# Optimization experiments

Measured on AMD Instinct MI355X. Metric: run time of the kernel, lower is better.

Reference implementation:

```python
import jax, jax.numpy as jnp
import numpy as np

N_WORDS = 30000
EMB_DIM = 784  # 28*28
MAT_DIM = 28
BATCH = 1024
SEQ_LEN = 64


def setup_inputs() -> dict:
    key = jax.random.key(0)
    k_sent, k_tab = jax.random.split(key)
    # token ids in [0, n_words]; row 0 is the neutral (identity) / padding element
    sent = jax.random.randint(k_sent, (BATCH, SEQ_LEN), 0, N_WORDS + 1, dtype=jnp.int32).astype(jnp.int64)
    eye_flat = jnp.eye(MAT_DIM, dtype=jnp.float32).reshape(-1)
    # 'identity' init strategy: identity + small gaussian noise (scale kept small for stability of long products)
    table = eye_flat + 0.01 * jax.random.normal(k_tab, (N_WORDS + 1, EMB_DIM), dtype=jnp.float32)
    table = table.at[0].set(eye_flat)  # neutral element at padding_idx=0
    return {"sent": sent, "table": table}


def reference(sent, table):
    # sent: [B, S] int ids; table: [n_words+1, d*d]
    B, S = sent.shape
    d = MAT_DIM
    word_mats = table[sent].reshape(B, S, d, d)  # embedding lookup + unflatten
    # CMOW: continual multiplication cur = cur @ W_i, sequential over seq dim
    init = word_mats[:, 0]                      # [B, d, d]
    rest = jnp.moveaxis(word_mats[:, 1:], 1, 0)  # [S-1, B, d, d]

    def step(cur, w):
        return jnp.matmul(cur, w), None

    cur, _ = jax.lax.scan(step, init, rest)
    return cur.reshape(B, d * d)  # flatten matrix back to embedding
```

## Files before the change

### kernel.cpp

```cpp
#include <hip/hip_runtime.h>
#include <stdint.h>

#define SEQ 64
#define D 28
#define EMB 784
#define NW 4
#define CH 16
#define BUFF 832
#define SCRW 36

typedef float float4v __attribute__((ext_vector_type(4)));
typedef __bf16 bf16x8 __attribute__((ext_vector_type(8)));

union FragU { unsigned u[4]; bf16x8 v; };

__device__ __forceinline__ unsigned fbits(float x) { union { float f; unsigned u; } t; t.f = x; return t.u; }
__device__ __forceinline__ float fof(unsigned u) { union { unsigned u; float f; } t; t.u = u; return t.f; }

struct HL4 { unsigned h01, h23, l01, l23; };
__device__ __forceinline__ HL4 hilo4(float x0, float x1, float x2, float x3) {
    unsigned u0 = fbits(x0), u1 = fbits(x1), u2 = fbits(x2), u3 = fbits(x3);
    HL4 r;
    r.h01 = (u0 >> 16) | (u1 & 0xFFFF0000u);
    r.h23 = (u2 >> 16) | (u3 & 0xFFFF0000u);
    unsigned l0 = fbits(x0 - fof(u0 & 0xFFFF0000u));
    unsigned l1 = fbits(x1 - fof(u1 & 0xFFFF0000u));
    unsigned l2 = fbits(x2 - fof(u2 & 0xFFFF0000u));
    unsigned l3 = fbits(x3 - fof(u3 & 0xFFFF0000u));
    r.l01 = (l0 >> 16) | (l1 & 0xFFFF0000u);
    r.l23 = (l2 >> 16) | (l3 & 0xFFFF0000u);
    return r;
}

__device__ __forceinline__ void dma_row(const float* grow, float* lbuf, int lane)
{
    const char* g16 = (const char*)grow + lane * 16;
    const char* g4  = (const char*)grow + 3072 + lane * 4;
    char* l = (char*)lbuf;
    __builtin_amdgcn_global_load_lds((const __attribute__((address_space(1))) void*)(g16),
                                     (__attribute__((address_space(3))) void*)(l), 16, 0, 0);
    __builtin_amdgcn_global_load_lds((const __attribute__((address_space(1))) void*)(g16 + 1024),
                                     (__attribute__((address_space(3))) void*)(l + 1024), 16, 0, 0);
    __builtin_amdgcn_global_load_lds((const __attribute__((address_space(1))) void*)(g16 + 2048),
                                     (__attribute__((address_space(3))) void*)(l + 2048), 16, 0, 0);
    __builtin_amdgcn_global_load_lds((const __attribute__((address_space(1))) void*)(g4),
                                     (__attribute__((address_space(3))) void*)(l + 3072), 4, 0, 0);
}

template<int STRIDE>
__device__ __forceinline__ void stepT(const float* a0, const float* a1,
                                      float4v acc[2][2], bool q3)
{
    float av[2][2][4];
#pragma unroll
    for (int t = 0; t < 4; ++t)
#pragma unroll
        for (int Ro = 0; Ro < 2; ++Ro) {
            av[Ro][0][t] = a0[t * STRIDE + 16 * Ro];
            av[Ro][1][t] = a1[t * STRIDE + 16 * Ro];
        }
#pragma unroll
    for (int Ro = 0; Ro < 2; ++Ro)
#pragma unroll
        for (int t = 0; t < 4; ++t)
            av[Ro][1][t] = q3 ? 0.f : av[Ro][1][t];

    FragU Af[2][2];
#pragma unroll
    for (int Ro = 0; Ro < 2; ++Ro)
#pragma unroll
        for (int KB = 0; KB < 2; ++KB) {
            HL4 h = hilo4(av[Ro][KB][0], av[Ro][KB][1], av[Ro][KB][2], av[Ro][KB][3]);
            Af[Ro][KB].u[0] = h.h01; Af[Ro][KB].u[1] = h.h23;
            Af[Ro][KB].u[2] = h.l01; Af[Ro][KB].u[3] = h.l23;
        }

    FragU Bd[2][2], B2[2][2];
#pragma unroll
    for (int KB = 0; KB < 2; ++KB)
#pragma unroll
        for (int Co = 0; Co < 2; ++Co) {
            HL4 h = hilo4(acc[KB][Co][0], acc[KB][Co][1], acc[KB][Co][2], acc[KB][Co][3]);
            Bd[KB][Co].u[0] = h.h01; Bd[KB][Co].u[1] = h.h23;
            Bd[KB][Co].u[2] = h.h01; Bd[KB][Co].u[3] = h.h23;
            B2[KB][Co].u[0] = h.l01; B2[KB][Co].u[1] = h.l23;
            B2[KB][Co].u[2] = 0u;    B2[KB][Co].u[3] = 0u;
        }

#pragma unroll
    for (int Ro = 0; Ro < 2; ++Ro)
#pragma unroll
        for (int Co = 0; Co < 2; ++Co) {
            float4v d = {0.f, 0.f, 0.f, 0.f};
#pragma unroll
            for (int KB = 0; KB < 2; ++KB) {
                d = __builtin_amdgcn_mfma_f32_16x16x32_bf16(Af[Ro][KB].v, Bd[KB][Co].v, d, 0, 0, 0);
                d = __builtin_amdgcn_mfma_f32_16x16x32_bf16(Af[Ro][KB].v, B2[KB][Co].v, d, 0, 0, 0);
            }
            acc[Ro][Co] = d;
        }
}

__global__ __launch_bounds__(NW * 64, 4) void w2m_fusedT3(
    const int* __restrict__ sent,
    const float* __restrict__ table,
    float* __restrict__ out)
{
    __shared__ float SH[NW * 3 * BUFF] __attribute__((aligned(16)));
    const int lane = threadIdx.x & 63;
    const int wid  = threadIdx.x >> 6;
    const int b = blockIdx.x;
    const int c = lane & 15;
    const int quad = lane >> 4;
    const bool q3 = (quad == 3);
    const int qc = q3 ? 2 : quad;

    float* B0 = &SH[wid * 3 * BUFF];
    float* B1 = B0 + BUFF;
    float* B2b = B0 + 2 * BUFF;

    const int myidx = sent[b * SEQ + CH * wid + (lane & (CH - 1))];
    int jl[CH];
#pragma unroll
    for (int j = 0; j < CH; ++j) jl[j] = __builtin_amdgcn_readlane(myidx, j);

    dma_row(table + (size_t)jl[0] * EMB, B0, lane);
    dma_row(table + (size_t)jl[1] * EMB, B1, lane);
    dma_row(table + (size_t)jl[2] * EMB, B2b, lane);
    __builtin_amdgcn_s_waitcnt(0x0078);

    float4v acc[2][2];
#pragma unroll
    for (int R = 0; R < 2; ++R)
#pragma unroll
        for (int Cc = 0; Cc < 2; ++Cc) {
            int rcl = 16 * Cc + c; if (rcl > 27) rcl = 27;
            acc[R][Cc] = *(const float4v*)&B0[rcl * D + 16 * R + 4 * quad];
        }

    const float* a00 = B0  + 4 * quad * D + c;
    const float* a10 = B0  + (16 + 4 * qc) * D + c;
    const float* a01 = B1  + 4 * quad * D + c;
    const float* a11 = B1  + (16 + 4 * qc) * D + c;
    const float* a02 = B2b + 4 * quad * D + c;
    const float* a12 = B2b + (16 + 4 * qc) * D + c;

#pragma unroll
    for (int j = 1; j < CH; ++j) {
        __builtin_amdgcn_s_waitcnt(0xC07F);
        const int jn = (j + 2 < CH) ? j + 2 : CH - 1;
        const int tb = (j + 2) % 3;
        float* nB = (tb == 0) ? B0 : (tb == 1) ? B1 : B2b;
        dma_row(table + (size_t)jl[jn] * EMB, nB, lane);

        __builtin_amdgcn_sched_barrier(0);
        __builtin_amdgcn_s_waitcnt(0x0078);
        __builtin_amdgcn_sched_barrier(0);

        const int cb = j % 3;
        if (cb == 0)      stepT<D>(a00, a10, acc, q3);
        else if (cb == 1) stepT<D>(a01, a11, acc, q3);
        else              stepT<D>(a02, a12, acc, q3);
    }

    __builtin_amdgcn_s_waitcnt(0x0070);
    __builtin_amdgcn_sched_barrier(0);
    float* SCR = B0;
#pragma unroll
    for (int R = 0; R < 2; ++R)
#pragma unroll
        for (int Cc = 0; Cc < 2; ++Cc)
#pragma unroll
            for (int i = 0; i < 4; ++i)
                SCR[(16 * R + 4 * quad + i) * SCRW + 16 * Cc + c] = acc[R][Cc][i];
    __syncthreads();

    const float* S3 = &SH[3 * 3 * BUFF];
#pragma unroll
    for (int R = 0; R < 2; ++R)
#pragma unroll
        for (int Cc = 0; Cc < 2; ++Cc)
            acc[R][Cc] = *(const float4v*)&S3[(16 * Cc + c) * SCRW + 16 * R + 4 * quad];

#pragma unroll
    for (int j = 2; j >= 0; --j) {
        const float* reg = &SH[j * 3 * BUFF];
        stepT<SCRW>(reg + 4 * quad * SCRW + c,
                    reg + (16 + 4 * quad) * SCRW + c, acc, q3);
    }

    if (wid == 0) {
        float* orow = out + (size_t)b * EMB;
#pragma unroll
        for (int R = 0; R < 2; ++R)
#pragma unroll
            for (int Cc = 0; Cc < 2; ++Cc)
#pragma unroll
                for (int i = 0; i < 4; ++i) {
                    const int row = 16 * R + 4 * quad + i;
                    const int col = 16 * Cc + c;
                    if (row < D && col < D) orow[row * D + col] = acc[R][Cc][i];
                }
    }
}

extern "C" void kernel_launch(void* const* d_in, const int* in_sizes, int n_in,
                              void* d_out, int out_size, void* d_ws, size_t ws_size,
                              hipStream_t stream) {
    const int* sent = (const int*)d_in[0];
    const float* table = (const float*)d_in[1];
    float* out = (float*)d_out;
    const int batch = in_sizes[0] / SEQ;
    (void)d_ws; (void)ws_size;

    hipLaunchKernelGGL(w2m_fusedT3, dim3(batch), dim3(NW * 64), 0, stream,
                       sent, table, out);
}
```

Baseline: 153.3 us.

## Interleave two independent product chains per wave to break MFMA dependency

Each wave's 16-matrix chunk is split into two independent chains, the first eight and last eight matrices, with token loads interleaved so consecutive steps alternate between two accumulators. The two partial products are then combined through LDS before the existing cross-wave reduction. The aim is to hide MFMA and conversion latency in the serial matmul chain by giving the scheduler independent work. The cost is extra registers for the second accumulator and an additional LDS round-trip plus matmul at the end.

Result: no change. 154.0 us (+0.5%).

```diff
diff --git a/kernel.cpp b/kernel.cpp
--- a/kernel.cpp
+++ b/kernel.cpp
@@ -101,7 +101,7 @@
         }
 }
 
-__global__ __launch_bounds__(NW * 64, 4) void w2m_fusedT3(
+__global__ __launch_bounds__(NW * 64, 4) void w2m_fusedT3i(
     const int* __restrict__ sent,
     const float* __restrict__ table,
     float* __restrict__ out)
@@ -115,27 +115,28 @@
     const bool q3 = (quad == 3);
     const int qc = q3 ? 2 : quad;
 
-    float* B0 = &SH[wid * 3 * BUFF];
-    float* B1 = B0 + BUFF;
+    float* B0  = &SH[wid * 3 * BUFF];
+    float* B1  = B0 + BUFF;
     float* B2b = B0 + 2 * BUFF;
 
-    const int myidx = sent[b * SEQ + CH * wid + (lane & (CH - 1))];
-    int jl[CH];
-#pragma unroll
-    for (int j = 0; j < CH; ++j) jl[j] = __builtin_amdgcn_readlane(myidx, j);
-
-    dma_row(table + (size_t)jl[0] * EMB, B0, lane);
-    dma_row(table + (size_t)jl[1] * EMB, B1, lane);
-    dma_row(table + (size_t)jl[2] * EMB, B2b, lane);
+    const int myidx = sent[b * SEQ + CH * wid + (lane & 15)];
+    int jr[16];
+#pragma unroll
+    for (int s = 0; s < 16; ++s)
+        jr[s] = __builtin_amdgcn_readlane(myidx, (s & 1) * 8 + (s >> 1));
+
+    dma_row(table + (size_t)jr[0] * EMB, B0, lane);
+    dma_row(table + (size_t)jr[1] * EMB, B1, lane);
+    dma_row(table + (size_t)jr[2] * EMB, B2b, lane);
     __builtin_amdgcn_s_waitcnt(0x0078);
 
-    float4v acc[2][2];
+    float4v accA[2][2], accB[2][2];
 #pragma unroll
     for (int R = 0; R < 2; ++R)
 #pragma unroll
         for (int Cc = 0; Cc < 2; ++Cc) {
             int rcl = 16 * Cc + c; if (rcl > 27) rcl = 27;
-            acc[R][Cc] = *(const float4v*)&B0[rcl * D + 16 * R + 4 * quad];
+            accA[R][Cc] = *(const float4v*)&B0[rcl * D + 16 * R + 4 * quad];
         }
 
     const float* a00 = B0  + 4 * quad * D + c;
@@ -146,33 +147,59 @@
     const float* a12 = B2b + (16 + 4 * qc) * D + c;
 
 #pragma unroll
-    for (int j = 1; j < CH; ++j) {
+    for (int s = 1; s < 16; ++s) {
         __builtin_amdgcn_s_waitcnt(0xC07F);
-        const int jn = (j + 2 < CH) ? j + 2 : CH - 1;
-        const int tb = (j + 2) % 3;
+        const int sn = (s + 2 < 16) ? s + 2 : 15;
+        const int tb = (s + 2) % 3;
         float* nB = (tb == 0) ? B0 : (tb == 1) ? B1 : B2b;
-        dma_row(table + (size_t)jl[jn] * EMB, nB, lane);
+        dma_row(table + (size_t)jr[sn] * EMB, nB, lane);
 
         __builtin_amdgcn_sched_barrier(0);
         __builtin_amdgcn_s_waitcnt(0x0078);
         __builtin_amdgcn_sched_barrier(0);
 
-        const int cb = j % 3;
-        if (cb == 0)      stepT<D>(a00, a10, acc, q3);
-        else if (cb == 1) stepT<D>(a01, a11, acc, q3);
-        else              stepT<D>(a02, a12, acc, q3);
+        if (s == 1) {
+#pragma unroll
+            for (int R = 0; R < 2; ++R)
+#pragma unroll
+                for (int Cc = 0; Cc < 2; ++Cc) {
+                    int rcl = 16 * Cc + c; if (rcl > 27) rcl = 27;
+                    accB[R][Cc] = *(const float4v*)&B1[rcl * D + 16 * R + 4 * quad];
+                }
+        } else {
+            float4v (*acc)[2] = (s & 1) ? accB : accA;
+            const int cb = s % 3;
+            if (cb == 0)      stepT<D>(a00, a10, acc, q3);
+            else if (cb == 1) stepT<D>(a01, a11, acc, q3);
+            else              stepT<D>(a02, a12, acc, q3);
+        }
     }
 
     __builtin_amdgcn_s_waitcnt(0x0070);
     __builtin_amdgcn_sched_barrier(0);
     float* SCR = B0;
 #pragma unroll
+    for (int KB = 0; KB < 2; ++KB)
+#pragma unroll
+        for (int Co = 0; Co < 2; ++Co)
+#pragma unroll
+            for (int i = 0; i < 4; ++i)
+                SCR[(16 * Co + c) * SCRW + 16 * KB + 4 * quad + i] = accB[KB][Co][i];
+    __builtin_amdgcn_sched_barrier(0);
+    __builtin_amdgcn_s_waitcnt(0xC07F);
+    __builtin_amdgcn_sched_barrier(0);
+    stepT<SCRW>(SCR + 4 * quad * SCRW + c,
+                SCR + (16 + 4 * quad) * SCRW + c, accA, q3);
+
+    __builtin_amdgcn_s_waitcnt(0xC07F);
+    __builtin_amdgcn_sched_barrier(0);
+#pragma unroll
     for (int R = 0; R < 2; ++R)
 #pragma unroll
         for (int Cc = 0; Cc < 2; ++Cc)
 #pragma unroll
             for (int i = 0; i < 4; ++i)
-                SCR[(16 * R + 4 * quad + i) * SCRW + 16 * Cc + c] = acc[R][Cc][i];
+                SCR[(16 * R + 4 * quad + i) * SCRW + 16 * Cc + c] = accA[R][Cc][i];
     __syncthreads();
 
     const float* S3 = &SH[3 * 3 * BUFF];
@@ -180,13 +207,13 @@
     for (int R = 0; R < 2; ++R)
 #pragma unroll
         for (int Cc = 0; Cc < 2; ++Cc)
-            acc[R][Cc] = *(const float4v*)&S3[(16 * Cc + c) * SCRW + 16 * R + 4 * quad];
+            accA[R][Cc] = *(const float4v*)&S3[(16 * Cc + c) * SCRW + 16 * R + 4 * quad];
 
 #pragma unroll
     for (int j = 2; j >= 0; --j) {
         const float* reg = &SH[j * 3 * BUFF];
         stepT<SCRW>(reg + 4 * quad * SCRW + c,
-                    reg + (16 + 4 * quad) * SCRW + c, acc, q3);
+                    reg + (16 + 4 * quad) * SCRW + c, accA, q3);
     }
 
     if (wid == 0) {
@@ -199,7 +226,7 @@
                 for (int i = 0; i < 4; ++i) {
                     const int row = 16 * R + 4 * quad + i;
                     const int col = 16 * Cc + c;
-                    if (row < D && col < D) orow[row * D + col] = acc[R][Cc][i];
+                    if (row < D && col < D) orow[row * D + col] = accA[R][Cc][i];
                 }
     }
 }
@@ -213,6 +240,6 @@
     const int batch = in_sizes[0] / SEQ;
     (void)d_ws; (void)ws_size;
 
-    hipLaunchKernelGGL(w2m_fusedT3, dim3(batch), dim3(NW * 64), 0, stream,
+    hipLaunchKernelGGL(w2m_fusedT3i, dim3(batch), dim3(NW * 64), 0, stream,
                        sent, table, out);
 }
```

## Use fp16 MFMA on identity-shifted residuals and split sequence across 8 waves

Applied to the files above, without the earlier changes.

Replaces the bf16 hi/lo split-precision product (four MFMAs per tile) with a single fp16 MFMA per tile. Subtracting the identity from each word matrix lets the accumulator carry the exact identity term while only the small residual is multiplied at low precision. The sequence is split into 8 chunks of 8 across 8 waves, which gives more parallelism but a longer 7-step cross-wave reduction and double the LDS footprint. The risks are reduced fp16 precision on the accumulator operand and lower occupancy.

After: 148.1 us. -3.4%, faster.

```diff
diff --git a/kernel.cpp b/kernel.cpp
--- a/kernel.cpp
+++ b/kernel.cpp
@@ -4,33 +4,16 @@
 #define SEQ 64
 #define D 28
 #define EMB 784
-#define NW 4
-#define CH 16
+#define NW 8
+#define CH 8
 #define BUFF 832
 #define SCRW 36
 
 typedef float float4v __attribute__((ext_vector_type(4)));
-typedef __bf16 bf16x8 __attribute__((ext_vector_type(8)));
-
-union FragU { unsigned u[4]; bf16x8 v; };
+typedef _Float16 half8 __attribute__((ext_vector_type(8)));
 
 __device__ __forceinline__ unsigned fbits(float x) { union { float f; unsigned u; } t; t.f = x; return t.u; }
 __device__ __forceinline__ float fof(unsigned u) { union { unsigned u; float f; } t; t.u = u; return t.f; }
-
-struct HL4 { unsigned h01, h23, l01, l23; };
-__device__ __forceinline__ HL4 hilo4(float x0, float x1, float x2, float x3) {
-    unsigned u0 = fbits(x0), u1 = fbits(x1), u2 = fbits(x2), u3 = fbits(x3);
-    HL4 r;
-    r.h01 = (u0 >> 16) | (u1 & 0xFFFF0000u);
-    r.h23 = (u2 >> 16) | (u3 & 0xFFFF0000u);
-    unsigned l0 = fbits(x0 - fof(u0 & 0xFFFF0000u));
-    unsigned l1 = fbits(x1 - fof(u1 & 0xFFFF0000u));
-    unsigned l2 = fbits(x2 - fof(u2 & 0xFFFF0000u));
-    unsigned l3 = fbits(x3 - fof(u3 & 0xFFFF0000u));
-    r.l01 = (l0 >> 16) | (l1 & 0xFFFF0000u);
-    r.l23 = (l2 >> 16) | (l3 & 0xFFFF0000u);
-    return r;
-}
 
 __device__ __forceinline__ void dma_row(const float* grow, float* lbuf, int lane)
 {
@@ -43,13 +26,15 @@
                                      (__attribute__((address_space(3))) void*)(l + 1024), 16, 0, 0);
     __builtin_amdgcn_global_load_lds((const __attribute__((address_space(1))) void*)(g16 + 2048),
                                      (__attribute__((address_space(3))) void*)(l + 2048), 16, 0, 0);
-    __builtin_amdgcn_global_load_lds((const __attribute__((address_space(1))) void*)(g4),
-                                     (__attribute__((address_space(3))) void*)(l + 3072), 4, 0, 0);
+    if (lane < 16)
+        __builtin_amdgcn_global_load_lds((const __attribute__((address_space(1))) void*)(g4),
+                                         (__attribute__((address_space(3))) void*)(l + 3072), 4, 0, 0);
 }
 
 template<int STRIDE>
-__device__ __forceinline__ void stepT(const float* a0, const float* a1,
-                                      float4v acc[2][2], bool q3)
+__device__ __forceinline__ void stepE(const float* a0, const float* a1,
+                                      float4v acc[2][2], bool q3,
+                                      const float dia[4])
 {
     float av[2][2][4];
 #pragma unroll
@@ -60,48 +45,43 @@
             av[Ro][1][t] = a1[t * STRIDE + 16 * Ro];
         }
 #pragma unroll
+    for (int t = 0; t < 4; ++t) {
+        av[0][0][t] -= dia[t];
+        av[1][1][t] -= dia[t];
+    }
+#pragma unroll
     for (int Ro = 0; Ro < 2; ++Ro)
 #pragma unroll
         for (int t = 0; t < 4; ++t)
             av[Ro][1][t] = q3 ? 0.f : av[Ro][1][t];
 
-    FragU Af[2][2];
+    half8 Av[2];
 #pragma unroll
     for (int Ro = 0; Ro < 2; ++Ro)
 #pragma unroll
-        for (int KB = 0; KB < 2; ++KB) {
-            HL4 h = hilo4(av[Ro][KB][0], av[Ro][KB][1], av[Ro][KB][2], av[Ro][KB][3]);
-            Af[Ro][KB].u[0] = h.h01; Af[Ro][KB].u[1] = h.h23;
-            Af[Ro][KB].u[2] = h.l01; Af[Ro][KB].u[3] = h.l23;
-        }
-
-    FragU Bd[2][2], B2[2][2];
-#pragma unroll
-    for (int KB = 0; KB < 2; ++KB)
-#pragma unroll
-        for (int Co = 0; Co < 2; ++Co) {
-            HL4 h = hilo4(acc[KB][Co][0], acc[KB][Co][1], acc[KB][Co][2], acc[KB][Co][3]);
-            Bd[KB][Co].u[0] = h.h01; Bd[KB][Co].u[1] = h.h23;
-            Bd[KB][Co].u[2] = h.h01; Bd[KB][Co].u[3] = h.h23;
-            B2[KB][Co].u[0] = h.l01; B2[KB][Co].u[1] = h.l23;
-            B2[KB][Co].u[2] = 0u;    B2[KB][Co].u[3] = 0u;
+        for (int t = 0; t < 4; ++t) {
+            Av[Ro][t]     = (_Float16)av[Ro][0][t];
+            Av[Ro][4 + t] = (_Float16)av[Ro][1][t];
+        }
+
+    half8 Bv[2];
+#pragma unroll
+    for (int Co = 0; Co < 2; ++Co)
+#pragma unroll
+        for (int t = 0; t < 4; ++t) {
+            Bv[Co][t]     = (_Float16)acc[0][Co][t];
+            Bv[Co][4 + t] = (_Float16)acc[1][Co][t];
         }
 
 #pragma unroll
     for (int Ro = 0; Ro < 2; ++Ro)
 #pragma unroll
-        for (int Co = 0; Co < 2; ++Co) {
-            float4v d = {0.f, 0.f, 0.f, 0.f};
-#pragma unroll
-            for (int KB = 0; KB < 2; ++KB) {
-                d = __builtin_amdgcn_mfma_f32_16x16x32_bf16(Af[Ro][KB].v, Bd[KB][Co].v, d, 0, 0, 0);
-                d = __builtin_amdgcn_mfma_f32_16x16x32_bf16(Af[Ro][KB].v, B2[KB][Co].v, d, 0, 0, 0);
-            }
-            acc[Ro][Co] = d;
-        }
-}
-
-__global__ __launch_bounds__(NW * 64, 4) void w2m_fusedT3(
+        for (int Co = 0; Co < 2; ++Co)
+            acc[Ro][Co] = __builtin_amdgcn_mfma_f32_16x16x32_f16(
+                Av[Ro], Bv[Co], acc[Ro][Co], 0, 0, 0);
+}
+
+__global__ __launch_bounds__(NW * 64, 4) void w2m_fused8(
     const int* __restrict__ sent,
     const float* __restrict__ table,
     float* __restrict__ out)
@@ -115,18 +95,23 @@
     const bool q3 = (quad == 3);
     const int qc = q3 ? 2 : quad;
 
-    float* B0 = &SH[wid * 3 * BUFF];
-    float* B1 = B0 + BUFF;
+    float dia[4];
+#pragma unroll
+    for (int t = 0; t < 4; ++t)
+        dia[t] = ((c >> 2) == quad && (c & 3) == t) ? 1.f : 0.f;
+
+    float* B0  = &SH[wid * 3 * BUFF];
+    float* B1  = B0 + BUFF;
     float* B2b = B0 + 2 * BUFF;
 
-    const int myidx = sent[b * SEQ + CH * wid + (lane & (CH - 1))];
-    int jl[CH];
-#pragma unroll
-    for (int j = 0; j < CH; ++j) jl[j] = __builtin_amdgcn_readlane(myidx, j);
-
-    dma_row(table + (size_t)jl[0] * EMB, B0, lane);
-    dma_row(table + (size_t)jl[1] * EMB, B1, lane);
-    dma_row(table + (size_t)jl[2] * EMB, B2b, lane);
+    const int myidx = sent[b * SEQ + CH * wid + (lane & 7)];
+    int jr[CH];
+#pragma unroll
+    for (int s = 0; s < CH; ++s) jr[s] = __builtin_amdgcn_readlane(myidx, s);
+
+    dma_row(table + (size_t)jr[0] * EMB, B0, lane);
+    dma_row(table + (size_t)jr[1] * EMB, B1, lane);
+    dma_row(table + (size_t)jr[2] * EMB, B2b, lane);
     __builtin_amdgcn_s_waitcnt(0x0078);
 
     float4v acc[2][2];
@@ -146,24 +131,25 @@
     const float* a12 = B2b + (16 + 4 * qc) * D + c;
 
 #pragma unroll
-    for (int j = 1; j < CH; ++j) {
-        __builtin_amdgcn_s_waitcnt(0xC07F);
-        const int jn = (j + 2 < CH) ? j + 2 : CH - 1;
-        const int tb = (j + 2) % 3;
-        float* nB = (tb == 0) ? B0 : (tb == 1) ? B1 : B2b;
-        dma_row(table + (size_t)jl[jn] * EMB, nB, lane);
-
+    for (int s = 1; s < CH; ++s) {
+        if (s <= 5) {
+            __builtin_amdgcn_s_waitcnt(0xC07F);
+            const int tb = (s + 2) % 3;
+            float* nB = (tb == 0) ? B0 : (tb == 1) ? B1 : B2b;
+            dma_row(table + (size_t)jr[s + 2] * EMB, nB, lane);
+        }
         __builtin_amdgcn_sched_barrier(0);
-        __builtin_amdgcn_s_waitcnt(0x0078);
+        if (s <= 5)      __builtin_amdgcn_s_waitcnt(0x0078);
+        else if (s == 6) __builtin_amdgcn_s_waitcnt(0x0074);
+        else             __builtin_amdgcn_s_waitcnt(0x0070);
         __builtin_amdgcn_sched_barrier(0);
 
-        const int cb = j % 3;
-        if (cb == 0)      stepT<D>(a00, a10, acc, q3);
-        else if (cb == 1) stepT<D>(a01, a11, acc, q3);
-        else              stepT<D>(a02, a12, acc, q3);
-    }
-
-    __builtin_amdgcn_s_waitcnt(0x0070);
+        const int cb = s % 3;
+        if (cb == 0)      stepE<D>(a00, a10, acc, q3, dia);
+        else if (cb == 1) stepE<D>(a01, a11, acc, q3, dia);
+        else              stepE<D>(a02, a12, acc, q3, dia);
+    }
+
     __builtin_amdgcn_sched_barrier(0);
     float* SCR = B0;
 #pragma unroll
@@ -175,18 +161,18 @@
                 SCR[(16 * R + 4 * quad + i) * SCRW + 16 * Cc + c] = acc[R][Cc][i];
     __syncthreads();
 
-    const float* S3 = &SH[3 * 3 * BUFF];
+    const float* S7 = &SH[7 * 3 * BUFF];
 #pragma unroll
     for (int R = 0; R < 2; ++R)
 #pragma unroll
         for (int Cc = 0; Cc < 2; ++Cc)
-            acc[R][Cc] = *(const float4v*)&S3[(16 * Cc + c) * SCRW + 16 * R + 4 * quad];
-
-#pragma unroll
-    for (int j = 2; j >= 0; --j) {
+            acc[R][Cc] = *(const float4v*)&S7[(16 * Cc + c) * SCRW + 16 * R + 4 * quad];
+
+#pragma unroll
+    for (int j = 6; j >= 0; --j) {
         const float* reg = &SH[j * 3 * BUFF];
-        stepT<SCRW>(reg + 4 * quad * SCRW + c,
-                    reg + (16 + 4 * quad) * SCRW + c, acc, q3);
+        stepE<SCRW>(reg + 4 * quad * SCRW + c,
+                    reg + (16 + 4 * quad) * SCRW + c, acc, q3, dia);
     }
 
     if (wid == 0) {
@@ -213,6 +199,6 @@
     const int batch = in_sizes[0] / SEQ;
     (void)d_ws; (void)ws_size;
 
-    hipLaunchKernelGGL(w2m_fusedT3, dim3(batch), dim3(NW * 64), 0, stream,
+    hipLaunchKernelGGL(w2m_fused8, dim3(batch), dim3(NW * 64), 0, stream,
                        sent, table, out);
 }
```
